# Performance work log

Measured on AMD Instinct MI355X. Metric: run time of the kernel, lower is better.

## Reference

```python
import jax, jax.numpy as jnp
import numpy as np
import math

B, T, HID, H = 2, 2048, 2048, 16
D = HID // H  # 128
START_RATIO, RECENT_RATIO = 0.1, 0.25
ROPE_THETA = 10000.0


def setup_inputs() -> dict:
    key = jax.random.key(0)
    k1, k2, k3, k4, k5 = jax.random.split(key, 5)
    hidden_states = jax.random.normal(k1, (B, T, HID), jnp.float32)
    causal = jnp.tril(jnp.ones((T, T), bool))
    attention_mask = jnp.broadcast_to(
        jnp.where(causal, 0.0, jnp.finfo(jnp.float32).min)[None, None], (B, 1, T, T)
    )
    q_w = 0.02 * jax.random.normal(k2, (HID, HID), jnp.float32)
    k_w = 0.02 * jax.random.normal(k3, (HID, HID), jnp.float32)
    v_w = 0.02 * jax.random.normal(k4, (HID, HID), jnp.float32)
    o_w = 0.02 * jax.random.normal(k5, (HID, HID), jnp.float32)
    return dict(hidden_states=hidden_states, attention_mask=attention_mask,
                q_w=q_w, k_w=k_w, v_w=v_w, o_w=o_w)


def _rotate_half(x):
    x1, x2 = x[..., : D // 2], x[..., D // 2:]
    return jnp.concatenate([-x2, x1], axis=-1)


def _local_cam_mask(V, A_bar, recent_budget):
    # V: [B,H,K,D], A_bar: [B,H,K]
    K = V.shape[-2]
    m = recent_budget
    if m <= 0 or m >= K:
        return V
    evict_idx = max(0, min(K - m - 1, K - 1))
    ws = max(0, K - m)
    avg_window = jnp.clip(jnp.mean(A_bar[..., ws:], axis=-1), 1e-6, None)  # [B,H]
    prob = jnp.clip(A_bar[..., evict_idx] / avg_window, 0.0, 1.0)
    prob = jnp.nan_to_num(prob, nan=0.0, posinf=1.0, neginf=0.0)
    mask = jax.lax.stop_gradient(
        jax.random.bernoulli(jax.random.key(42), prob).astype(V.dtype)
    )  # [B,H]
    v_e = V[..., evict_idx, :] * mask[..., None] / m  # [B,H,D]
    return V.at[..., ws:, :].add(v_e[..., None, :])


def reference(hidden_states, attention_mask, q_w, k_w, v_w, o_w):
    MIN = jnp.finfo(hidden_states.dtype).min
    hs = jnp.nan_to_num(hidden_states, nan=0.0, posinf=1e4, neginf=-1e4)

    def proj(w):
        return (hs @ w.T).reshape(B, T, H, D).transpose(0, 2, 1, 3)  # [B,H,T,D]

    Q, K, V = proj(q_w), proj(k_w), proj(v_w)

    # rotary embedding (standard Llama)
    pos = jnp.arange(T, dtype=jnp.float32)
    inv_freq = 1.0 / (ROPE_THETA ** (jnp.arange(0, D, 2, dtype=jnp.float32) / D))
    freqs = pos[:, None] * inv_freq[None, :]  # [T, D/2]
    emb = jnp.concatenate([freqs, freqs], axis=-1)  # [T, D]
    cos, sin = jnp.cos(emb)[None, None], jnp.sin(emb)[None, None]
    Q = Q * cos + _rotate_half(Q) * sin
    K = K * cos + _rotate_half(K) * sin

    scores = jnp.einsum('bhtd,bhkd->bhtk', Q, K) / math.sqrt(D) + attention_mask
    scores = jnp.nan_to_num(scores, nan=MIN, posinf=MIN, neginf=MIN)
    attn = jax.nn.softmax(scores, axis=-1)  # [B,H,T,T]

    # first call: A_bar = detached last-row attention
    A_bar = jax.lax.stop_gradient(attn[..., -1, :])  # [B,H,T]

    k_len = T
    sb = max(0, min(int(START_RATIO * k_len), k_len))
    rb = max(0, min(int(RECENT_RATIO * k_len), k_len - sb))
    V = _local_cam_mask(V, A_bar, rb)

    attn_out = jnp.einsum('bhtk,bhkd->bhtd', attn, V)
    out = attn_out.transpose(0, 2, 1, 3).reshape(B, T, HID)
    return out @ o_w.T
```

## Files before the change

kernel.cpp:

```cpp
#include <hip/hip_runtime.h>
#include <cstdint>
#include <cstddef>


#define DEVINL __device__ __forceinline__

typedef float  f32x4  __attribute__((ext_vector_type(4)));
typedef __bf16 bf16x8 __attribute__((ext_vector_type(8)));

DEVINL float bf2f(unsigned short u){
  unsigned int x = ((unsigned int)u) << 16;
  return __builtin_bit_cast(float, x);
}
DEVINL unsigned short f2bf(float f){
  unsigned int u = __builtin_bit_cast(unsigned int, f);
  u = (u + 0x7fffu + ((u >> 16) & 1u)) >> 16;
  return (unsigned short)u;
}

DEVINL void load_lds16(const void* g, void* l){
  __builtin_amdgcn_global_load_lds(
      (const __attribute__((address_space(1))) void*)g,
      (__attribute__((address_space(3))) void*)l, 16, 0, 0);
}

__global__ void cvt_bf16_kernel(const float* __restrict__ s,
                                unsigned short* __restrict__ d, int n4){
  int i = blockIdx.x * 256 + threadIdx.x;
  if (i >= n4) return;
  float4 v = reinterpret_cast<const float4*>(s)[i];
  uint2 o;
  o.x = (unsigned)f2bf(v.x) | ((unsigned)f2bf(v.y) << 16);
  o.y = (unsigned)f2bf(v.z) | ((unsigned)f2bf(v.w) << 16);
  reinterpret_cast<uint2*>(d)[i] = o;
}

template<int MODE>
__global__ __launch_bounds__(256, 2)
void gemm_bt_kernel(const unsigned short* __restrict__ A,
                    const unsigned short* __restrict__ B,
                    void* __restrict__ out, int M, int N, int K){
  __shared__ unsigned short As[128 * 64];
  __shared__ unsigned short Bs[128 * 64];
  const int tid = threadIdx.x, wave = tid >> 6, lane = tid & 63;
  const int m16 = lane & 15, quad = lane >> 4;
  const int m0 = blockIdx.y * 128, n0 = blockIdx.x * 128;
  const int wm = wave >> 1, wn = wave & 1;

  f32x4 acc[4][4] = {};

  for (int k0 = 0; k0 < K; k0 += 64){
    __syncthreads();
    #pragma unroll
    for (int i = 0; i < 4; ++i){
      int r  = wave * 32 + i * 8 + (lane >> 3);
      int c8 = (lane & 7) ^ (r & 7);
      load_lds16(A + (size_t)(m0 + r) * K + k0 + c8 * 8, &As[(wave * 32 + i * 8) * 64]);
      load_lds16(B + (size_t)(n0 + r) * K + k0 + c8 * 8, &Bs[(wave * 32 + i * 8) * 64]);
    }
    __syncthreads();
    #pragma unroll
    for (int kc = 0; kc < 2; ++kc){
      bf16x8 af[4], bfr[4];
      #pragma unroll
      for (int mt = 0; mt < 4; ++mt){
        int r = wm * 64 + mt * 16 + m16;
        af[mt] = *reinterpret_cast<const bf16x8*>(&As[(r * 8 + ((quad + 4 * kc) ^ (r & 7))) * 8]);
      }
      #pragma unroll
      for (int nt = 0; nt < 4; ++nt){
        int r = wn * 64 + nt * 16 + m16;
        bfr[nt] = *reinterpret_cast<const bf16x8*>(&Bs[(r * 8 + ((quad + 4 * kc) ^ (r & 7))) * 8]);
      }
      #pragma unroll
      for (int mt = 0; mt < 4; ++mt)
        #pragma unroll
        for (int nt = 0; nt < 4; ++nt)
          acc[mt][nt] = __builtin_amdgcn_mfma_f32_16x16x32_bf16(af[mt], bfr[nt], acc[mt][nt], 0, 0, 0);
    }
  }

  #pragma unroll
  for (int mt = 0; mt < 4; ++mt){
    #pragma unroll
    for (int nt = 0; nt < 4; ++nt){
      #pragma unroll
      for (int reg = 0; reg < 4; ++reg){
        int m = m0 + wm * 64 + mt * 16 + quad * 4 + reg;
        int n = n0 + wn * 64 + nt * 16 + m16;
        float v = acc[mt][nt][reg];
        if constexpr (MODE == 0){
          ((unsigned short*)out)[((((size_t)(m >> 11)) * 16 + (n >> 7)) * 2048 + (m & 2047)) * 128 + (n & 127)] = f2bf(v);
        } else if constexpr (MODE == 1){
          ((unsigned short*)out)[((((size_t)(m >> 11)) * 16 + (n >> 7)) * 128 + (n & 127)) * 2048 + (m & 2047)] = f2bf(v);
        } else {
          ((float*)out)[(size_t)m * N + n] = v;
        }
      }
    }
  }
}

__global__ void rope_kernel(unsigned short* __restrict__ Q, unsigned short* __restrict__ K){
  int gid = blockIdx.x * 256 + threadIdx.x;
  int d2 = gid & 63;
  int t  = (gid >> 6) & 2047;
  int bh = (gid >> 17) & 31;
  unsigned short* P = (gid >> 22) ? K : Q;
  size_t base = ((size_t)bh * 2048 + t) * 128;
  float x1 = bf2f(P[base + d2]);
  float x2 = bf2f(P[base + d2 + 64]);
  float inv = expf(-(float)d2 * 0.14391156606007266f);
  float fr = (float)t * inv;
  float sn, cs;
  sincosf(fr, &sn, &cs);
  P[base + d2]      = f2bf(x1 * cs - x2 * sn);
  P[base + d2 + 64] = f2bf(x2 * cs + x1 * sn);
}

DEVINL unsigned int rotl32(unsigned int x, int r){ return (x << r) | (x >> (32 - r)); }

__device__ float threefry_u01(int i){
  unsigned int c0 = (i < 16) ? (unsigned)i : (unsigned)(i - 16);
  unsigned int c1 = (i < 16) ? (unsigned)(i + 16) : (unsigned)i;
  bool hi = (i >= 16);
  unsigned int k0 = 0u, k1 = 42u, k2 = 0x1BD11BDAu ^ k0 ^ k1;
  unsigned int ks[3] = {k0, k1, k2};
  unsigned int x0 = c0 + k0, x1 = c1 + k1;
  const int R0[4] = {13, 15, 26, 6}, R1[4] = {17, 29, 16, 24};
  #pragma unroll
  for (int r = 0; r < 5; ++r){
    const int* RR = (r & 1) ? R1 : R0;
    #pragma unroll
    for (int j = 0; j < 4; ++j){ x0 += x1; x1 = rotl32(x1, RR[j]); x1 ^= x0; }
    x0 += ks[(r + 1) % 3];
    x1 += ks[(r + 2) % 3] + (unsigned)(r + 1);
  }
  unsigned int bits = hi ? x1 : x0;
  return __builtin_bit_cast(float, (bits >> 9) | 0x3f800000u) - 1.0f;
}

DEVINL float wred_max(float v){
  #pragma unroll
  for (int m = 1; m < 64; m <<= 1) v = fmaxf(v, __shfl_xor(v, m));
  return v;
}
DEVINL float wred_sum(float v){
  #pragma unroll
  for (int m = 1; m < 64; m <<= 1) v += __shfl_xor(v, m);
  return v;
}

__global__ __launch_bounds__(256)
void cam_kernel(const unsigned short* __restrict__ Q,
                const unsigned short* __restrict__ K,
                unsigned short* __restrict__ Vt){
  const int bh = blockIdx.x, tid = threadIdx.x;
  __shared__ float qv[128];
  __shared__ float redm[4], reds[4], redw[4];
  __shared__ float e1535s;
  __shared__ float bc0;
  if (tid < 128) qv[tid] = bf2f(Q[((size_t)bh * 2048 + 2047) * 128 + tid]);
  __syncthreads();

  float sc[8];
  float smax = -1e30f;
  #pragma unroll
  for (int j = 0; j < 8; ++j){
    int k = tid + j * 256;
    const uint4* kr4 = reinterpret_cast<const uint4*>(K + ((size_t)bh * 2048 + k) * 128);
    float acc = 0.f;
    #pragma unroll
    for (int c = 0; c < 16; ++c){
      uint4 pk = kr4[c];
      acc += qv[c * 8 + 0] * bf2f((unsigned short)(pk.x & 0xffff));
      acc += qv[c * 8 + 1] * bf2f((unsigned short)(pk.x >> 16));
      acc += qv[c * 8 + 2] * bf2f((unsigned short)(pk.y & 0xffff));
      acc += qv[c * 8 + 3] * bf2f((unsigned short)(pk.y >> 16));
      acc += qv[c * 8 + 4] * bf2f((unsigned short)(pk.z & 0xffff));
      acc += qv[c * 8 + 5] * bf2f((unsigned short)(pk.z >> 16));
      acc += qv[c * 8 + 6] * bf2f((unsigned short)(pk.w & 0xffff));
      acc += qv[c * 8 + 7] * bf2f((unsigned short)(pk.w >> 16));
    }
    sc[j] = acc * 0.08838834764831843f;
    smax = fmaxf(smax, sc[j]);
  }
  int wave = tid >> 6, lane = tid & 63;
  float wm = wred_max(smax);
  if (lane == 0) redm[wave] = wm;
  __syncthreads();
  float M = fmaxf(fmaxf(redm[0], redm[1]), fmaxf(redm[2], redm[3]));
  float tsum = 0.f, wsum = 0.f;
  #pragma unroll
  for (int j = 0; j < 8; ++j){
    int k = tid + j * 256;
    float e = expf(sc[j] - M);
    if (k == 1535) e1535s = e;
    tsum += e;
    if (k >= 1536) wsum += e;
  }
  tsum = wred_sum(tsum); wsum = wred_sum(wsum);
  if (lane == 0){ reds[wave] = tsum; redw[wave] = wsum; }
  __syncthreads();
  if (tid == 0){
    float sum = reds[0] + reds[1] + reds[2] + reds[3];
    float wsm = redw[0] + redw[1] + redw[2] + redw[3];
    float abar = e1535s / sum;
    float avg  = fmaxf(wsm / (512.f * sum), 1e-6f);
    float pr   = abar / avg;
    pr = fminf(fmaxf(pr, 0.f), 1.f);
    float u = threefry_u01(bh);
    bc0 = (u < pr) ? (1.f / 512.f) : 0.f;
  }
  __syncthreads();
  float ves = bc0;
  if (ves != 0.f){
    for (int idx = tid; idx < 128 * 64; idx += 256){
      int d = idx >> 6, c = idx & 63;
      unsigned short* row = Vt + ((size_t)bh * 128 + d) * 2048;
      float ve = bf2f(row[1535]) * ves;
      uint4* p = reinterpret_cast<uint4*>(row + 1536) + c;
      uint4 pk = *p;
      unsigned short h0 = f2bf(bf2f((unsigned short)(pk.x & 0xffff)) + ve);
      unsigned short h1 = f2bf(bf2f((unsigned short)(pk.x >> 16)) + ve);
      unsigned short h2 = f2bf(bf2f((unsigned short)(pk.y & 0xffff)) + ve);
      unsigned short h3 = f2bf(bf2f((unsigned short)(pk.y >> 16)) + ve);
      unsigned short h4 = f2bf(bf2f((unsigned short)(pk.z & 0xffff)) + ve);
      unsigned short h5 = f2bf(bf2f((unsigned short)(pk.z >> 16)) + ve);
      unsigned short h6 = f2bf(bf2f((unsigned short)(pk.w & 0xffff)) + ve);
      unsigned short h7 = f2bf(bf2f((unsigned short)(pk.w >> 16)) + ve);
      pk.x = (unsigned)h0 | ((unsigned)h1 << 16);
      pk.y = (unsigned)h2 | ((unsigned)h3 << 16);
      pk.z = (unsigned)h4 | ((unsigned)h5 << 16);
      pk.w = (unsigned)h6 | ((unsigned)h7 << 16);
      *p = pk;
    }
  }
}

__global__ __launch_bounds__(256, 2)
void flash_kernel(const unsigned short* __restrict__ Q,
                  const unsigned short* __restrict__ K,
                  const unsigned short* __restrict__ Vt,
                  unsigned short* __restrict__ AO){
  __shared__ unsigned short smem[32768];
  unsigned short* Qs = smem;
  unsigned short* Ks = smem + 16384;
  unsigned short* Vs = smem + 24576;
  const int qt = blockIdx.x, bh = blockIdx.y;
  const int tid = threadIdx.x, wave = tid >> 6, lane = tid & 63;
  const int m16 = lane & 15, quad = lane >> 4;
  unsigned short* Pw = smem + wave * 2048;

  {
    size_t qbase = ((size_t)bh * 2048 + (size_t)qt * 128) * 128;
    #pragma unroll
    for (int i = 0; i < 8; ++i){
      int r   = wave * 32 + i * 4 + (lane >> 4);
      int c16 = (lane & 15) ^ (r & 15);
      load_lds16(Q + qbase + (size_t)r * 128 + c16 * 8, &Qs[(wave * 32 + i * 4) * 128]);
    }
  }
  __syncthreads();
  bf16x8 qf[2][4];
  #pragma unroll
  for (int mt = 0; mt < 2; ++mt)
    #pragma unroll
    for (int kc = 0; kc < 4; ++kc){
      int r = wave * 32 + mt * 16 + m16;
      qf[mt][kc] = *reinterpret_cast<const bf16x8*>(&Qs[(r * 16 + ((quad + 4 * kc) ^ (r & 15))) * 8]);
    }

  f32x4 oacc[2][8] = {};
  f32x4 mstat[2], lstat[2] = {};
  #pragma unroll
  for (int a = 0; a < 2; ++a){
    f32x4 v = {-1e30f, -1e30f, -1e30f, -1e30f};
    mstat[a] = v;
  }

  const int nkt = 2 * qt + 2;
  for (int kt = 0; kt < nkt; ++kt){
    __syncthreads();
    {
      size_t kb = ((size_t)bh * 2048 + (size_t)kt * 64) * 128;
      #pragma unroll
      for (int i = 0; i < 4; ++i){
        int r   = wave * 16 + i * 4 + (lane >> 4);
        int c16 = (lane & 15) ^ (r & 15);
        load_lds16(K + kb + (size_t)r * 128 + c16 * 8, &Ks[(wave * 16 + i * 4) * 128]);
      }
      #pragma unroll
      for (int i = 0; i < 4; ++i){
        int r  = wave * 32 + i * 8 + (lane >> 3);
        int c8 = (lane & 7) ^ (r & 7);
        load_lds16(Vt + ((size_t)bh * 128 + r) * 2048 + (size_t)kt * 64 + c8 * 8,
                   &Vs[(wave * 32 + i * 8) * 64]);
      }
    }
    __syncthreads();

    f32x4 s[2][4] = {};
    #pragma unroll
    for (int kc = 0; kc < 4; ++kc){
      bf16x8 kf[4];
      #pragma unroll
      for (int nt = 0; nt < 4; ++nt){
        int r = nt * 16 + m16;
        kf[nt] = *reinterpret_cast<const bf16x8*>(&Ks[(r * 16 + ((quad + 4 * kc) ^ (r & 15))) * 8]);
      }
      #pragma unroll
      for (int mt = 0; mt < 2; ++mt)
        #pragma unroll
        for (int nt = 0; nt < 4; ++nt)
          s[mt][nt] = __builtin_amdgcn_mfma_f32_16x16x32_bf16(qf[mt][kc], kf[nt], s[mt][nt], 0, 0, 0);
    }

    const bool domask = (kt >= 2 * qt);
    #pragma unroll
    for (int mt = 0; mt < 2; ++mt)
      #pragma unroll
      for (int nt = 0; nt < 4; ++nt)
        #pragma unroll
        for (int reg = 0; reg < 4; ++reg){
          float v = s[mt][nt][reg] * 0.08838834764831843f;
          if (domask){
            int key = kt * 64 + nt * 16 + m16;
            int qr  = qt * 128 + wave * 32 + mt * 16 + quad * 4 + reg;
            if (key > qr) v = -1e30f;
          }
          s[mt][nt][reg] = v;
        }

    #pragma unroll
    for (int mt = 0; mt < 2; ++mt){
      #pragma unroll
      for (int reg = 0; reg < 4; ++reg){
        float rm = fmaxf(fmaxf(s[mt][0][reg], s[mt][1][reg]),
                         fmaxf(s[mt][2][reg], s[mt][3][reg]));
        rm = fmaxf(rm, __shfl_xor(rm, 1));
        rm = fmaxf(rm, __shfl_xor(rm, 2));
        rm = fmaxf(rm, __shfl_xor(rm, 4));
        rm = fmaxf(rm, __shfl_xor(rm, 8));
        float mold = mstat[mt][reg];
        float mnew = fmaxf(mold, rm);
        float alpha = expf(mold - mnew);
        float rs = 0.f;
        #pragma unroll
        for (int nt = 0; nt < 4; ++nt){
          float p = expf(s[mt][nt][reg] - mnew);
          s[mt][nt][reg] = p;
          rs += p;
        }
        rs += __shfl_xor(rs, 1);
        rs += __shfl_xor(rs, 2);
        rs += __shfl_xor(rs, 4);
        rs += __shfl_xor(rs, 8);
        lstat[mt][reg] = lstat[mt][reg] * alpha + rs;
        mstat[mt][reg] = mnew;
        #pragma unroll
        for (int dt = 0; dt < 8; ++dt) oacc[mt][dt][reg] *= alpha;
      }
    }

    #pragma unroll
    for (int mt = 0; mt < 2; ++mt)
      #pragma unroll
      for (int nt = 0; nt < 4; ++nt)
        #pragma unroll
        for (int reg = 0; reg < 4; ++reg){
          int r   = mt * 16 + quad * 4 + reg;
          int col = nt * 16 + m16;
          Pw[(r * 8 + ((col >> 3) ^ (r & 7))) * 8 + (col & 7)] = f2bf(s[mt][nt][reg]);
        }

    #pragma unroll
    for (int kc = 0; kc < 2; ++kc){
      bf16x8 pf[2];
      #pragma unroll
      for (int mt = 0; mt < 2; ++mt){
        int r = mt * 16 + m16;
        pf[mt] = *reinterpret_cast<const bf16x8*>(&Pw[(r * 8 + ((quad + 4 * kc) ^ (r & 7))) * 8]);
      }
      #pragma unroll
      for (int dt = 0; dt < 8; ++dt){
        int r = dt * 16 + m16;
        bf16x8 vf = *reinterpret_cast<const bf16x8*>(&Vs[(r * 8 + ((quad + 4 * kc) ^ (r & 7))) * 8]);
        #pragma unroll
        for (int mt = 0; mt < 2; ++mt)
          oacc[mt][dt] = __builtin_amdgcn_mfma_f32_16x16x32_bf16(pf[mt], vf, oacc[mt][dt], 0, 0, 0);
      }
    }
  }

  const int b = bh >> 4, h = bh & 15;
  #pragma unroll
  for (int mt = 0; mt < 2; ++mt){
    #pragma unroll
    for (int reg = 0; reg < 4; ++reg){
      int t = qt * 128 + wave * 32 + mt * 16 + quad * 4 + reg;
      float inv = 1.0f / lstat[mt][reg];
      size_t obase = ((size_t)b * 2048 + t) * 2048 + (size_t)h * 128;
      #pragma unroll
      for (int dt = 0; dt < 8; ++dt)
        AO[obase + dt * 16 + m16] = f2bf(oacc[mt][dt][reg] * inv);
    }
  }
}

extern "C" void kernel_launch(void* const* d_in, const int* in_sizes, int n_in,
                              void* d_out, int out_size, void* d_ws, size_t ws_size,
                              hipStream_t stream){
  const float* hs = (const float*)d_in[0];
  const float* qw = (const float*)d_in[2];
  const float* kw = (const float*)d_in[3];
  const float* vw = (const float*)d_in[4];
  const float* ow = (const float*)d_in[5];

  char* ws = (char*)d_ws;
  const size_t MB = 1ull << 20;
  unsigned short* hsb = (unsigned short*)(ws);
  unsigned short* qwb = (unsigned short*)(ws + 16 * MB);
  unsigned short* kwb = (unsigned short*)(ws + 24 * MB);
  unsigned short* vwb = (unsigned short*)(ws + 32 * MB);
  unsigned short* owb = (unsigned short*)(ws + 40 * MB);
  unsigned short* Qb  = (unsigned short*)(ws + 48 * MB);
  unsigned short* Kb  = (unsigned short*)(ws + 64 * MB);
  unsigned short* Vtb = (unsigned short*)(ws + 80 * MB);
  unsigned short* AOb = (unsigned short*)(ws + 96 * MB);

  cvt_bf16_kernel<<<8192, 256, 0, stream>>>(hs, hsb, 2097152);
  cvt_bf16_kernel<<<4096, 256, 0, stream>>>(qw, qwb, 1048576);
  cvt_bf16_kernel<<<4096, 256, 0, stream>>>(kw, kwb, 1048576);
  cvt_bf16_kernel<<<4096, 256, 0, stream>>>(vw, vwb, 1048576);
  cvt_bf16_kernel<<<4096, 256, 0, stream>>>(ow, owb, 1048576);

  dim3 g(16, 32);
  gemm_bt_kernel<0><<<g, 256, 0, stream>>>(hsb, qwb, Qb,  4096, 2048, 2048);
  gemm_bt_kernel<0><<<g, 256, 0, stream>>>(hsb, kwb, Kb,  4096, 2048, 2048);
  gemm_bt_kernel<1><<<g, 256, 0, stream>>>(hsb, vwb, Vtb, 4096, 2048, 2048);

  rope_kernel<<<32768, 256, 0, stream>>>(Qb, Kb);
  cam_kernel<<<32, 256, 0, stream>>>(Qb, Kb, Vtb);
  flash_kernel<<<dim3(16, 32), 256, 0, stream>>>(Qb, Kb, Vtb, AOb);

  gemm_bt_kernel<2><<<g, 256, 0, stream>>>(AOb, owb, d_out, 4096, 2048, 2048);
}
```

Measured before the change: 546.6 us.

## Pair causal query tiles per block with double-buffered KV and exp2 softmax

The flash kernel now gives each block two 64-row query tiles, g and 31-g, so every block does about the same amount of causal work. K/V tiles are double-buffered in LDS so the next tile loads while the current one is processed. The softmax scale and log2(e) are folded into Q during RoPE, which lets the flash and CAM kernels use exp2f and drop the per-score multiply. The five conversion launches are merged into one kernel; the cost is more LDS per block and bf16 rounding of the pre-scaled Q.

```diff
diff --git a/kernel.cpp b/kernel.cpp
--- a/kernel.cpp
+++ b/kernel.cpp
@@ -24,15 +24,27 @@
       (__attribute__((address_space(3))) void*)l, 16, 0, 0);
 }
 
-__global__ void cvt_bf16_kernel(const float* __restrict__ s,
-                                unsigned short* __restrict__ d, int n4){
+#define QSCALE 0.127517432f
+
+__global__ void cvt_all_kernel(const float* __restrict__ hs, const float* __restrict__ qw,
+                               const float* __restrict__ kw, const float* __restrict__ vw,
+                               const float* __restrict__ ow,
+                               unsigned short* __restrict__ hsb, unsigned short* __restrict__ qwb,
+                               unsigned short* __restrict__ kwb, unsigned short* __restrict__ vwb,
+                               unsigned short* __restrict__ owb){
   int i = blockIdx.x * 256 + threadIdx.x;
-  if (i >= n4) return;
-  float4 v = reinterpret_cast<const float4*>(s)[i];
+  const float* s; unsigned short* d; int off;
+  if (i < 2097152){ s = hs; d = hsb; off = i; }
+  else {
+    int j = i - 2097152; int w = j >> 20; off = j & 1048575;
+    s = (w == 0) ? qw : (w == 1) ? kw : (w == 2) ? vw : ow;
+    d = (w == 0) ? qwb : (w == 1) ? kwb : (w == 2) ? vwb : owb;
+  }
+  float4 v = reinterpret_cast<const float4*>(s)[off];
   uint2 o;
   o.x = (unsigned)f2bf(v.x) | ((unsigned)f2bf(v.y) << 16);
   o.y = (unsigned)f2bf(v.z) | ((unsigned)f2bf(v.w) << 16);
-  reinterpret_cast<uint2*>(d)[i] = o;
+  reinterpret_cast<uint2*>(d)[off] = o;
 }
 
 template<int MODE>
@@ -106,7 +118,9 @@
   int d2 = gid & 63;
   int t  = (gid >> 6) & 2047;
   int bh = (gid >> 17) & 31;
-  unsigned short* P = (gid >> 22) ? K : Q;
+  int isK = gid >> 22;
+  unsigned short* P = isK ? K : Q;
+  float sc = isK ? 1.0f : QSCALE;
   size_t base = ((size_t)bh * 2048 + t) * 128;
   float x1 = bf2f(P[base + d2]);
   float x2 = bf2f(P[base + d2 + 64]);
@@ -114,8 +128,8 @@
   float fr = (float)t * inv;
   float sn, cs;
   sincosf(fr, &sn, &cs);
-  P[base + d2]      = f2bf(x1 * cs - x2 * sn);
-  P[base + d2 + 64] = f2bf(x2 * cs + x1 * sn);
+  P[base + d2]      = f2bf((x1 * cs - x2 * sn) * sc);
+  P[base + d2 + 64] = f2bf((x2 * cs + x1 * sn) * sc);
 }
 
 DEVINL unsigned int rotl32(unsigned int x, int r){ return (x << r) | (x >> (32 - r)); }
@@ -182,7 +196,7 @@
       acc += qv[c * 8 + 6] * bf2f((unsigned short)(pk.w & 0xffff));
       acc += qv[c * 8 + 7] * bf2f((unsigned short)(pk.w >> 16));
     }
-    sc[j] = acc * 0.08838834764831843f;
+    sc[j] = acc;
     smax = fmaxf(smax, sc[j]);
   }
   int wave = tid >> 6, lane = tid & 63;
@@ -194,7 +208,7 @@
   #pragma unroll
   for (int j = 0; j < 8; ++j){
     int k = tid + j * 256;
-    float e = expf(sc[j] - M);
+    float e = exp2f(sc[j] - M);
     if (k == 1535) e1535s = e;
     tsum += e;
     if (k >= 1536) wsum += e;
@@ -243,169 +257,156 @@
                   const unsigned short* __restrict__ K,
                   const unsigned short* __restrict__ Vt,
                   unsigned short* __restrict__ AO){
-  __shared__ unsigned short smem[32768];
-  unsigned short* Qs = smem;
-  unsigned short* Ks = smem + 16384;
-  unsigned short* Vs = smem + 24576;
-  const int qt = blockIdx.x, bh = blockIdx.y;
+  __shared__ unsigned short Qs[64 * 128];
+  __shared__ unsigned short Ks0[64 * 128];
+  __shared__ unsigned short Vs0[128 * 64];
+  __shared__ unsigned short Ks1[64 * 128];
+  __shared__ unsigned short Vs1[128 * 64];
+  const int g = blockIdx.x, bh = blockIdx.y;
   const int tid = threadIdx.x, wave = tid >> 6, lane = tid & 63;
   const int m16 = lane & 15, quad = lane >> 4;
-  unsigned short* Pw = smem + wave * 2048;
-
-  {
-    size_t qbase = ((size_t)bh * 2048 + (size_t)qt * 128) * 128;
-    #pragma unroll
-    for (int i = 0; i < 8; ++i){
-      int r   = wave * 32 + i * 4 + (lane >> 4);
+  const int qt1 = g, qt2 = 31 - g;
+  const int nkt = 32 - g;
+  unsigned short* Pw = Qs + wave * 2048;
+
+  auto stageQ = [&](int qt){
+    size_t qb = ((size_t)bh * 2048 + (size_t)qt * 64) * 128;
+    #pragma unroll
+    for (int i = 0; i < 4; ++i){
+      int r   = wave * 16 + i * 4 + (lane >> 4);
       int c16 = (lane & 15) ^ (r & 15);
-      load_lds16(Q + qbase + (size_t)r * 128 + c16 * 8, &Qs[(wave * 32 + i * 4) * 128]);
-    }
-  }
-  __syncthreads();
-  bf16x8 qf[2][4];
-  #pragma unroll
-  for (int mt = 0; mt < 2; ++mt)
+      load_lds16(Q + qb + (size_t)r * 128 + c16 * 8, &Qs[(wave * 16 + i * 4) * 128]);
+    }
+  };
+  auto readQf = [&](bf16x8 (&qf)[4]){
+    int r = wave * 16 + m16;
+    #pragma unroll
+    for (int kc = 0; kc < 4; ++kc)
+      qf[kc] = *reinterpret_cast<const bf16x8*>(&Qs[(r * 16 + ((quad + 4 * kc) ^ (r & 15))) * 8]);
+  };
+  auto stageKV = [&](int kt, unsigned short* Ks, unsigned short* Vs){
+    size_t kb = ((size_t)bh * 2048 + (size_t)kt * 64) * 128;
+    #pragma unroll
+    for (int i = 0; i < 4; ++i){
+      int r   = wave * 16 + i * 4 + (lane >> 4);
+      int c16 = (lane & 15) ^ (r & 15);
+      load_lds16(K + kb + (size_t)r * 128 + c16 * 8, &Ks[(wave * 16 + i * 4) * 128]);
+    }
+    size_t vb = (size_t)bh * 128 * 2048 + (size_t)kt * 64;
+    #pragma unroll
+    for (int i = 0; i < 4; ++i){
+      int r  = wave * 32 + i * 8 + (lane >> 3);
+      int c8 = (lane & 7) ^ (r & 7);
+      load_lds16(Vt + vb + (size_t)r * 2048 + c8 * 8, &Vs[(wave * 32 + i * 8) * 64]);
+    }
+  };
+
+  bf16x8 qf1[4], qf2[4];
+  stageQ(qt1);
+  __syncthreads();
+  readQf(qf1);
+  __syncthreads();
+  stageQ(qt2);
+  __syncthreads();
+  readQf(qf2);
+
+  f32x4 o1[8] = {}, o2[8] = {};
+  f32x4 m1, m2, l1 = {}, l2 = {};
+  { f32x4 v = {-1e30f, -1e30f, -1e30f, -1e30f}; m1 = v; m2 = v; }
+
+  auto process = [&](bf16x8 (&qf)[4], f32x4& mst, f32x4& lst, f32x4 (&oacc)[8],
+                     const unsigned short* Ks, const unsigned short* Vs, bool diag){
+    f32x4 s[4] = {};
     #pragma unroll
     for (int kc = 0; kc < 4; ++kc){
-      int r = wave * 32 + mt * 16 + m16;
-      qf[mt][kc] = *reinterpret_cast<const bf16x8*>(&Qs[(r * 16 + ((quad + 4 * kc) ^ (r & 15))) * 8]);
-    }
-
-  f32x4 oacc[2][8] = {};
-  f32x4 mstat[2], lstat[2] = {};
-  #pragma unroll
-  for (int a = 0; a < 2; ++a){
-    f32x4 v = {-1e30f, -1e30f, -1e30f, -1e30f};
-    mstat[a] = v;
-  }
-
-  const int nkt = 2 * qt + 2;
-  for (int kt = 0; kt < nkt; ++kt){
-    __syncthreads();
-    {
-      size_t kb = ((size_t)bh * 2048 + (size_t)kt * 64) * 128;
-      #pragma unroll
-      for (int i = 0; i < 4; ++i){
-        int r   = wave * 16 + i * 4 + (lane >> 4);
-        int c16 = (lane & 15) ^ (r & 15);
-        load_lds16(K + kb + (size_t)r * 128 + c16 * 8, &Ks[(wave * 16 + i * 4) * 128]);
-      }
-      #pragma unroll
-      for (int i = 0; i < 4; ++i){
-        int r  = wave * 32 + i * 8 + (lane >> 3);
-        int c8 = (lane & 7) ^ (r & 7);
-        load_lds16(Vt + ((size_t)bh * 128 + r) * 2048 + (size_t)kt * 64 + c8 * 8,
-                   &Vs[(wave * 32 + i * 8) * 64]);
-      }
-    }
-    __syncthreads();
-
-    f32x4 s[2][4] = {};
-    #pragma unroll
-    for (int kc = 0; kc < 4; ++kc){
-      bf16x8 kf[4];
       #pragma unroll
       for (int nt = 0; nt < 4; ++nt){
         int r = nt * 16 + m16;
-        kf[nt] = *reinterpret_cast<const bf16x8*>(&Ks[(r * 16 + ((quad + 4 * kc) ^ (r & 15))) * 8]);
-      }
-      #pragma unroll
-      for (int mt = 0; mt < 2; ++mt)
-        #pragma unroll
-        for (int nt = 0; nt < 4; ++nt)
-          s[mt][nt] = __builtin_amdgcn_mfma_f32_16x16x32_bf16(qf[mt][kc], kf[nt], s[mt][nt], 0, 0, 0);
-    }
-
-    const bool domask = (kt >= 2 * qt);
-    #pragma unroll
-    for (int mt = 0; mt < 2; ++mt)
+        bf16x8 kf = *reinterpret_cast<const bf16x8*>(&Ks[(r * 16 + ((quad + 4 * kc) ^ (r & 15))) * 8]);
+        s[nt] = __builtin_amdgcn_mfma_f32_16x16x32_bf16(qf[kc], kf, s[nt], 0, 0, 0);
+      }
+    }
+    if (diag){
+      int lrow = wave * 16 + quad * 4;
       #pragma unroll
       for (int nt = 0; nt < 4; ++nt)
         #pragma unroll
-        for (int reg = 0; reg < 4; ++reg){
-          float v = s[mt][nt][reg] * 0.08838834764831843f;
-          if (domask){
-            int key = kt * 64 + nt * 16 + m16;
-            int qr  = qt * 128 + wave * 32 + mt * 16 + quad * 4 + reg;
-            if (key > qr) v = -1e30f;
-          }
-          s[mt][nt][reg] = v;
-        }
-
-    #pragma unroll
-    for (int mt = 0; mt < 2; ++mt){
+        for (int reg = 0; reg < 4; ++reg)
+          if (nt * 16 + m16 > lrow + reg) s[nt][reg] = -1e30f;
+    }
+    #pragma unroll
+    for (int reg = 0; reg < 4; ++reg){
+      float rm = fmaxf(fmaxf(s[0][reg], s[1][reg]), fmaxf(s[2][reg], s[3][reg]));
+      rm = fmaxf(rm, __shfl_xor(rm, 1));
+      rm = fmaxf(rm, __shfl_xor(rm, 2));
+      rm = fmaxf(rm, __shfl_xor(rm, 4));
+      rm = fmaxf(rm, __shfl_xor(rm, 8));
+      float mold = mst[reg];
+      float mnew = fmaxf(mold, rm);
+      float alpha = exp2f(mold - mnew);
+      float rs = 0.f;
+      #pragma unroll
+      for (int nt = 0; nt < 4; ++nt){
+        float p = exp2f(s[nt][reg] - mnew);
+        s[nt][reg] = p;
+        rs += p;
+      }
+      rs += __shfl_xor(rs, 1);
+      rs += __shfl_xor(rs, 2);
+      rs += __shfl_xor(rs, 4);
+      rs += __shfl_xor(rs, 8);
+      lst[reg] = lst[reg] * alpha + rs;
+      mst[reg] = mnew;
+      #pragma unroll
+      for (int dt = 0; dt < 8; ++dt) oacc[dt][reg] *= alpha;
+    }
+    #pragma unroll
+    for (int nt = 0; nt < 4; ++nt)
       #pragma unroll
       for (int reg = 0; reg < 4; ++reg){
-        float rm = fmaxf(fmaxf(s[mt][0][reg], s[mt][1][reg]),
-                         fmaxf(s[mt][2][reg], s[mt][3][reg]));
-        rm = fmaxf(rm, __shfl_xor(rm, 1));
-        rm = fmaxf(rm, __shfl_xor(rm, 2));
-        rm = fmaxf(rm, __shfl_xor(rm, 4));
-        rm = fmaxf(rm, __shfl_xor(rm, 8));
-        float mold = mstat[mt][reg];
-        float mnew = fmaxf(mold, rm);
-        float alpha = expf(mold - mnew);
-        float rs = 0.f;
-        #pragma unroll
-        for (int nt = 0; nt < 4; ++nt){
-          float p = expf(s[mt][nt][reg] - mnew);
-          s[mt][nt][reg] = p;
-          rs += p;
-        }
-        rs += __shfl_xor(rs, 1);
-        rs += __shfl_xor(rs, 2);
-        rs += __shfl_xor(rs, 4);
-        rs += __shfl_xor(rs, 8);
-        lstat[mt][reg] = lstat[mt][reg] * alpha + rs;
-        mstat[mt][reg] = mnew;
-        #pragma unroll
-        for (int dt = 0; dt < 8; ++dt) oacc[mt][dt][reg] *= alpha;
-      }
-    }
-
-    #pragma unroll
-    for (int mt = 0; mt < 2; ++mt)
-      #pragma unroll
-      for (int nt = 0; nt < 4; ++nt)
-        #pragma unroll
-        for (int reg = 0; reg < 4; ++reg){
-          int r   = mt * 16 + quad * 4 + reg;
-          int col = nt * 16 + m16;
-          Pw[(r * 8 + ((col >> 3) ^ (r & 7))) * 8 + (col & 7)] = f2bf(s[mt][nt][reg]);
-        }
-
+        int r   = quad * 4 + reg;
+        int col = nt * 16 + m16;
+        Pw[(r * 8 + ((col >> 3) ^ (r & 7))) * 8 + (col & 7)] = f2bf(s[nt][reg]);
+      }
     #pragma unroll
     for (int kc = 0; kc < 2; ++kc){
-      bf16x8 pf[2];
-      #pragma unroll
-      for (int mt = 0; mt < 2; ++mt){
-        int r = mt * 16 + m16;
-        pf[mt] = *reinterpret_cast<const bf16x8*>(&Pw[(r * 8 + ((quad + 4 * kc) ^ (r & 7))) * 8]);
-      }
+      bf16x8 pf = *reinterpret_cast<const bf16x8*>(&Pw[(m16 * 8 + ((quad + 4 * kc) ^ (m16 & 7))) * 8]);
       #pragma unroll
       for (int dt = 0; dt < 8; ++dt){
         int r = dt * 16 + m16;
         bf16x8 vf = *reinterpret_cast<const bf16x8*>(&Vs[(r * 8 + ((quad + 4 * kc) ^ (r & 7))) * 8]);
-        #pragma unroll
-        for (int mt = 0; mt < 2; ++mt)
-          oacc[mt][dt] = __builtin_amdgcn_mfma_f32_16x16x32_bf16(pf[mt], vf, oacc[mt][dt], 0, 0, 0);
-      }
-    }
+        oacc[dt] = __builtin_amdgcn_mfma_f32_16x16x32_bf16(pf, vf, oacc[dt], 0, 0, 0);
+      }
+    }
+  };
+
+  stageKV(0, Ks0, Vs0);
+  for (int base = 0; base < nkt; base += 2){
+    __syncthreads();
+    if (base + 1 < nkt) stageKV(base + 1, Ks1, Vs1);
+    process(qf2, m2, l2, o2, Ks0, Vs0, base == nkt - 1);
+    if (base <= g) process(qf1, m1, l1, o1, Ks0, Vs0, base == g);
+    if (base + 1 >= nkt) break;
+    __syncthreads();
+    if (base + 2 < nkt) stageKV(base + 2, Ks0, Vs0);
+    process(qf2, m2, l2, o2, Ks1, Vs1, base + 1 == nkt - 1);
+    if (base + 1 <= g) process(qf1, m1, l1, o1, Ks1, Vs1, base + 1 == g);
   }
 
   const int b = bh >> 4, h = bh & 15;
-  #pragma unroll
-  for (int mt = 0; mt < 2; ++mt){
+  auto epi = [&](int qt, f32x4& lst, f32x4 (&oacc)[8]){
     #pragma unroll
     for (int reg = 0; reg < 4; ++reg){
-      int t = qt * 128 + wave * 32 + mt * 16 + quad * 4 + reg;
-      float inv = 1.0f / lstat[mt][reg];
-      size_t obase = ((size_t)b * 2048 + t) * 2048 + (size_t)h * 128;
+      int t = qt * 64 + wave * 16 + quad * 4 + reg;
+      float inv = 1.0f / lst[reg];
+      size_t ob = ((size_t)b * 2048 + t) * 2048 + (size_t)h * 128;
       #pragma unroll
       for (int dt = 0; dt < 8; ++dt)
-        AO[obase + dt * 16 + m16] = f2bf(oacc[mt][dt][reg] * inv);
-    }
-  }
+        AO[ob + dt * 16 + m16] = f2bf(oacc[dt][reg] * inv);
+    }
+  };
+  epi(qt1, l1, o1);
+  epi(qt2, l2, o2);
 }
 
 extern "C" void kernel_launch(void* const* d_in, const int* in_sizes, int n_in,
@@ -429,11 +430,7 @@
   unsigned short* Vtb = (unsigned short*)(ws + 80 * MB);
   unsigned short* AOb = (unsigned short*)(ws + 96 * MB);
 
-  cvt_bf16_kernel<<<8192, 256, 0, stream>>>(hs, hsb, 2097152);
-  cvt_bf16_kernel<<<4096, 256, 0, stream>>>(qw, qwb, 1048576);
-  cvt_bf16_kernel<<<4096, 256, 0, stream>>>(kw, kwb, 1048576);
-  cvt_bf16_kernel<<<4096, 256, 0, stream>>>(vw, vwb, 1048576);
-  cvt_bf16_kernel<<<4096, 256, 0, stream>>>(ow, owb, 1048576);
+  cvt_all_kernel<<<24576, 256, 0, stream>>>(hs, qw, kw, vw, ow, hsb, qwb, kwb, vwb, owb);
 
   dim3 g(16, 32);
   gemm_bt_kernel<0><<<g, 256, 0, stream>>>(hsb, qwb, Qb,  4096, 2048, 2048);
```

Result: slower. 809.3 us (+48.1%).
